# Performance work log

Hardware: AMD Instinct MI355X
Metric: run time of the kernel (lower is better)

The kernel has to match this reference:

```python
import jax, jax.numpy as jnp
import numpy as np

DIM = 1024
EXP = 4           # expansion_factor
NUM_EXPERTS = 4
BATCH, SEQ = 4, 4096


def setup_inputs() -> dict:
    key = jax.random.key(0)
    ks = jax.random.split(key, 6)
    x = jax.random.normal(ks[0], (BATCH, SEQ, DIM), dtype=jnp.float32)
    token_mask = jax.random.randint(ks[1], (BATCH, SEQ), 0, NUM_EXPERTS, dtype=jnp.int32)
    hid = DIM * EXP
    s1 = 1.0 / np.sqrt(DIM)
    s2 = 1.0 / np.sqrt(hid)
    # nn.Linear layout: weight [out_features, in_features]
    w1 = jax.random.uniform(ks[2], (hid, DIM), minval=-s1, maxval=s1, dtype=jnp.float32)
    b1 = jax.random.uniform(ks[3], (hid,), minval=-s1, maxval=s1, dtype=jnp.float32)
    w2 = jax.random.uniform(ks[4], (DIM, hid), minval=-s2, maxval=s2, dtype=jnp.float32)
    b2 = jax.random.uniform(ks[5], (DIM,), minval=-s2, maxval=s2, dtype=jnp.float32)
    return {"x": x, "w1": w1, "b1": b1, "w2": w2, "b2": b2, "token_mask": token_mask}


def _nested_ffn(x, w1, b1, w2, b2, token_mask):
    dim = x.shape[-1]            # in_features of proj1
    out_dim = w2.shape[0]        # out_features of proj2 (== dim)
    # Expert m uses the first D_m = width >> (E-1-m) features (matryoshka nesting).
    # Expand (proj1): truncating input features to D_m and doing a full GEMM is
    # exactly equivalent to zeroing features >= D_m, so we mask then do one GEMM.
    d_in = dim >> (NUM_EXPERTS - 1 - token_mask)             # [B,S]
    in_mask = jnp.arange(dim) < d_in[..., None]              # [B,S,dim]
    h = jnp.einsum('bsd,fd->bsf', jnp.where(in_mask, x, jnp.zeros((), x.dtype)), w1) + b1
    h = jax.nn.gelu(h, approximate=False)                    # torch nn.GELU() default = erf
    # Contract (proj2): expert m produces only the first D_m outputs (incl. bias),
    # padded with zeros -> compute full GEMM then mask outputs.
    d_out = out_dim >> (NUM_EXPERTS - 1 - token_mask)        # [B,S]
    out_mask = jnp.arange(out_dim) < d_out[..., None]        # [B,S,out_dim]
    y = jnp.einsum('bsf,df->bsd', h, w2) + b2
    return jnp.where(out_mask, y, jnp.zeros((), y.dtype))


def reference(x, w1, b1, w2, b2, token_mask):
    return _nested_ffn(x, w1, b1, w2, b2, token_mask)
```

## Files before the change

### kernel.cpp

```cpp
#include <hip/hip_runtime.h>
#include <hip/hip_bf16.h>


typedef __bf16 bf16x8 __attribute__((ext_vector_type(8)));
typedef float f32x4 __attribute__((ext_vector_type(4)));

#define M_TOK   16384
#define DIM     1024
#define HID     4096

#define META_TK    40
#define META_BLK   64
#define META_MAP   256
#define META_RT    2560

__device__ inline unsigned int pk_bf16(float a, float b) {
  unsigned int r;
  asm("v_cvt_pk_bf16_f32 %0, %1, %2" : "=v"(r) : "v"(a), "v"(b));
  return r;
}

__device__ inline float gelu_f(float v) {
  float v2 = v * v;
  float w = v * fmaf(0.10294324f, v2, 2.30220830f);
  float e = __builtin_amdgcn_exp2f(-w);
  return v * __builtin_amdgcn_rcpf(1.0f + e);
}

__device__ inline void async_copy16(const void* g, void* s) {
  __builtin_amdgcn_global_load_lds(
      (const __attribute__((address_space(1))) unsigned int*)g,
      (__attribute__((address_space(3))) unsigned int*)s,
      16, 0, 0);
}

template<int ROWS, int LDK>
__device__ inline void stage_tile(const unsigned short* __restrict__ g,
                                  int row0, int k0, char* lds) {
  const char* gbase = (const char*)g;
  int tid = threadIdx.x;
#pragma unroll
  for (int i = 0; i < ROWS / 32; ++i) {
    int q = i * 256 + tid;
    int r = q >> 3;
    int c = q & 7;
    int gc = c ^ (r & 7);
    const void* gp = gbase + ((size_t)(row0 + r) * LDK + (size_t)k0 + gc * 8) * 2;
    async_copy16(gp, lds + (size_t)q * 16);
  }
}

__global__ __launch_bounds__(1024) void sortw_kernel(
    const int* __restrict__ tm,
    const float* __restrict__ w1,
    const float* __restrict__ w2,
    int* __restrict__ meta,
    unsigned short* __restrict__ w1b,
    unsigned short* __restrict__ w2b) {
  int tid = threadIdx.x;
  if (blockIdx.x != 0) {
    size_t i = (size_t)(blockIdx.x - 1) * 4096 + tid * 4;
    const float* src;
    unsigned short* dst;
    if (i < (size_t)HID * DIM) { src = w1; dst = w1b; }
    else { src = w2 - (size_t)HID * DIM; dst = w2b - (size_t)HID * DIM; }
    float4 v = *(const float4*)(src + i);
    uint2 o;
    o.x = pk_bf16(v.x, v.y);
    o.y = pk_bf16(v.z, v.w);
    *(uint2*)(dst + i) = o;
    return;
  }

  __shared__ unsigned short rt[16384];
  __shared__ unsigned int w01[16], w23[16];
  __shared__ int sbase[4];
  __shared__ int cb[128];
  int lane = tid & 63, wv = tid >> 6;

  int c0 = 0, c1 = 0, c2 = 0, c3 = 0;
  unsigned int epack = 0;
  int4 tv[4];
#pragma unroll
  for (int j = 0; j < 4; ++j)
    tv[j] = *(const int4*)(tm + tid * 16 + j * 4);
#pragma unroll
  for (int j = 0; j < 4; ++j) {
    int e;
    e = tv[j].x; epack |= (unsigned)e << (2 * (4 * j + 0)); c0 += (e == 0); c1 += (e == 1); c2 += (e == 2); c3 += (e == 3);
    e = tv[j].y; epack |= (unsigned)e << (2 * (4 * j + 1)); c0 += (e == 0); c1 += (e == 1); c2 += (e == 2); c3 += (e == 3);
    e = tv[j].z; epack |= (unsigned)e << (2 * (4 * j + 2)); c0 += (e == 0); c1 += (e == 1); c2 += (e == 2); c3 += (e == 3);
    e = tv[j].w; epack |= (unsigned)e << (2 * (4 * j + 3)); c0 += (e == 0); c1 += (e == 1); c2 += (e == 2); c3 += (e == 3);
  }
  unsigned int p01 = (unsigned)c0 | ((unsigned)c1 << 16);
  unsigned int p23 = (unsigned)c2 | ((unsigned)c3 << 16);
  unsigned int i01 = p01, i23 = p23;
#pragma unroll
  for (int s = 1; s < 64; s <<= 1) {
    unsigned int t0 = __shfl_up(i01, s, 64);
    unsigned int t1 = __shfl_up(i23, s, 64);
    if (lane >= s) { i01 += t0; i23 += t1; }
  }
  if (lane == 63) { w01[wv] = i01; w23[wv] = i23; }
  unsigned int e01 = i01 - p01, e23 = i23 - p23;
  __syncthreads();
  if (tid < 16) {
    unsigned int a = w01[tid], b = w23[tid];
    unsigned int ia = a, ib = b;
#pragma unroll
    for (int s = 1; s < 16; s <<= 1) {
      unsigned int t0 = __shfl_up(ia, s, 64);
      unsigned int t1 = __shfl_up(ib, s, 64);
      if (tid >= s) { ia += t0; ib += t1; }
    }
    w01[tid] = ia - a;
    w23[tid] = ib - b;
    if (tid == 15) {
      int t0 = (int)(ia & 0xFFFF), t1 = (int)(ia >> 16), t2 = (int)(ib & 0xFFFF);
      sbase[0] = 0; sbase[1] = t0; sbase[2] = t0 + t1; sbase[3] = t0 + t1 + t2;
    }
  }
  __syncthreads();
  int off0 = sbase[0] + (int)((w01[wv] & 0xFFFF) + (e01 & 0xFFFF));
  int off1 = sbase[1] + (int)((w01[wv] >> 16) + (e01 >> 16));
  int off2 = sbase[2] + (int)((w23[wv] & 0xFFFF) + (e23 & 0xFFFF));
  int off3 = sbase[3] + (int)((w23[wv] >> 16) + (e23 >> 16));
#pragma unroll
  for (int j = 0; j < 16; ++j) {
    int e = (epack >> (2 * j)) & 3;
    int t = tid * 16 + j;
    int pos = (e == 0) ? off0++ : (e == 1) ? off1++ : (e == 2) ? off2++ : off3++;
    rt[pos] = (unsigned short)(t | (e << 14));
  }
  __syncthreads();

  if (tid < 128) {
    int last = tid * 128 + 127;
    int e = (last >= sbase[1]) + (last >= sbase[2]) + (last >= sbase[3]);
    cb[tid] = 1 << e;
    meta[META_BLK + tid] = 128 << e;
  }
  __syncthreads();
  if (tid < 8) {
    int k = tid;
    int* map = meta + META_MAP + k * 128;
    int Tk = 0;
    for (int j = 0; j < 16; ++j) Tk += cb[k + 8 * j];
    meta[META_TK + k] = Tk;
    int pos = 0, zpos = Tk;
    for (int j = 0; j < 16; ++j) {
      int s = k + 8 * j;
      int n = cb[s];
      for (int c = 0; c < n; ++c) map[pos++] = s * 8 + c;
      for (int c = n; c < 8; ++c) map[zpos++] = s * 8 + c;
    }
  }
  int* rowtok = meta + META_RT;
#pragma unroll
  for (int j = 0; j < 16; ++j)
    rowtok[j * 1024 + tid] = (int)rt[j * 1024 + tid];
}

__global__ void prepx_kernel(const float* __restrict__ x,
                             const int* __restrict__ meta,
                             unsigned short* __restrict__ xb) {
  int b = blockIdx.x;
  int tid = threadIdx.x;
  int mt = meta[META_RT + b];
  int t = mt & 0x3FFF;
  int din = 128 << (mt >> 14);
  int kb = meta[META_BLK + (b >> 7)];
  int d = tid * 4;
  if (d < kb) {
    uint2 o; o.x = 0; o.y = 0;
    if (d < din) {
      float4 v = *(const float4*)(x + (size_t)t * DIM + d);
      o.x = pk_bf16(v.x, v.y);
      o.y = pk_bf16(v.z, v.w);
    }
    *(uint2*)(xb + (size_t)b * DIM + d) = o;
  }
}

__global__ __launch_bounds__(256) void gemm1_kernel(
    const unsigned short* __restrict__ A,
    const unsigned short* __restrict__ B,
    const float* __restrict__ bias,
    const int* __restrict__ meta,
    unsigned short* __restrict__ H)
{
  constexpr int K = DIM, N = HID;
  __shared__ char smem[65536];
  int tid = threadIdx.x;
  int lane = tid & 63, quad = lane >> 4, l15 = lane & 15;
  int wave = tid >> 6, wm = wave & 1, wn = wave >> 1;
  int Bk = blockIdx.x & 7, ord = blockIdx.x >> 3;
  int rowblk = 127 - (ord >> 2);
  int row0 = rowblk * 128, col0 = (Bk * 4 + (ord & 3)) * 128;
  int kmax = meta[META_BLK + rowblk];

  int chb = (quad ^ (l15 & 7)) << 4;

  f32x4 acc[4][4] = {};

  stage_tile<128, K>(A, row0, 0, smem);
  stage_tile<128, K>(B, col0, 0, smem + 16384);

  int nt = kmax >> 6;
  for (int t = 0; t < nt; ++t) {
    char* buf = smem + ((t & 1) << 15);
    if (t + 1 < nt) {
      char* nbuf = smem + (((t + 1) & 1) << 15);
      int kn = (t + 1) << 6;
      stage_tile<128, K>(A, row0, kn, nbuf);
      stage_tile<128, K>(B, col0, kn, nbuf + 16384);
      asm volatile("s_waitcnt vmcnt(8)" ::: "memory");
    } else {
      asm volatile("s_waitcnt vmcnt(0)" ::: "memory");
    }
    __builtin_amdgcn_s_barrier();
    char* As = buf;
    char* Bs = buf + 16384;
#pragma unroll
    for (int kk = 0; kk < 2; ++kk) {
      int xo = chb ^ (kk << 6);
      bf16x8 af[4], bg[4];
#pragma unroll
      for (int mt = 0; mt < 4; ++mt)
        af[mt] = *(const bf16x8*)(As + (wm * 64 + mt * 16 + l15) * 128 + xo);
#pragma unroll
      for (int nt2 = 0; nt2 < 4; ++nt2)
        bg[nt2] = *(const bf16x8*)(Bs + (wn * 64 + nt2 * 16 + l15) * 128 + xo);
#pragma unroll
      for (int mt = 0; mt < 4; ++mt)
#pragma unroll
        for (int nt2 = 0; nt2 < 4; ++nt2)
          acc[mt][nt2] = __builtin_amdgcn_mfma_f32_16x16x32_bf16(
              bg[nt2], af[mt], acc[mt][nt2], 0, 0, 0);
    }
    __builtin_amdgcn_s_barrier();
  }

  int t_base = row0 + wm * 64;
  int f_base = col0 + wn * 64;
#pragma unroll
  for (int nt2 = 0; nt2 < 4; ++nt2) {
    int f0 = f_base + nt2 * 16 + quad * 4;
    float4 bv = *(const float4*)(bias + f0);
#pragma unroll
    for (int mt = 0; mt < 4; ++mt) {
      int t = t_base + mt * 16 + l15;
      float v0 = gelu_f(acc[mt][nt2][0] + bv.x);
      float v1 = gelu_f(acc[mt][nt2][1] + bv.y);
      float v2 = gelu_f(acc[mt][nt2][2] + bv.z);
      float v3 = gelu_f(acc[mt][nt2][3] + bv.w);
      uint2 p;
      p.x = pk_bf16(v0, v1);
      p.y = pk_bf16(v2, v3);
      *(uint2*)(H + (size_t)t * N + f0) = p;
    }
  }
}

__global__ __launch_bounds__(256) void gemm2_kernel(
    const unsigned short* __restrict__ A,
    const unsigned short* __restrict__ B,
    const float* __restrict__ bias,
    const int* __restrict__ meta,
    float* __restrict__ out)
{
  constexpr int K = HID, N = DIM;
  int Bk = blockIdx.x & 7, ord = blockIdx.x >> 3;
  int Tk = meta[META_TK + Bk];
  int mp = meta[META_MAP + Bk * 128 + ord];
  int row0 = (mp >> 3) * 128, col0 = (mp & 7) * 128;
  const int* rowtok = meta + META_RT;
  int tid = threadIdx.x;

  if (ord >= Tk) {
    float4 z = make_float4(0.f, 0.f, 0.f, 0.f);
#pragma unroll
    for (int i = 0; i < 16; ++i) {
      int idx = i * 256 + tid;
      int r = idx >> 5;
      int col = (idx & 31) * 4;
      int t = rowtok[row0 + r] & 0x3FFF;
      *(float4*)(out + (size_t)t * N + col0 + col) = z;
    }
    return;
  }

  __shared__ char smem[65536];
  int lane = tid & 63, quad = lane >> 4, l15 = lane & 15;
  int wave = tid >> 6, wm = wave & 1, wn = wave >> 1;
  int chb = (quad ^ (l15 & 7)) << 4;

  f32x4 acc[4][4] = {};

  stage_tile<128, K>(A, row0, 0, smem);
  stage_tile<128, K>(B, col0, 0, smem + 16384);

  constexpr int NT = K >> 6;
  for (int t = 0; t < NT; ++t) {
    char* buf = smem + ((t & 1) << 15);
    if (t + 1 < NT) {
      char* nbuf = smem + (((t + 1) & 1) << 15);
      int kn = (t + 1) << 6;
      stage_tile<128, K>(A, row0, kn, nbuf);
      stage_tile<128, K>(B, col0, kn, nbuf + 16384);
      asm volatile("s_waitcnt vmcnt(8)" ::: "memory");
    } else {
      asm volatile("s_waitcnt vmcnt(0)" ::: "memory");
    }
    __builtin_amdgcn_s_barrier();
    char* As = buf;
    char* Bs = buf + 16384;
#pragma unroll
    for (int kk = 0; kk < 2; ++kk) {
      int xo = chb ^ (kk << 6);
      bf16x8 af[4], bg[4];
#pragma unroll
      for (int mt = 0; mt < 4; ++mt)
        af[mt] = *(const bf16x8*)(As + (wm * 64 + mt * 16 + l15) * 128 + xo);
#pragma unroll
      for (int nt2 = 0; nt2 < 4; ++nt2)
        bg[nt2] = *(const bf16x8*)(Bs + (wn * 64 + nt2 * 16 + l15) * 128 + xo);
#pragma unroll
      for (int mt = 0; mt < 4; ++mt)
#pragma unroll
        for (int nt2 = 0; nt2 < 4; ++nt2)
          acc[mt][nt2] = __builtin_amdgcn_mfma_f32_16x16x32_bf16(
              bg[nt2], af[mt], acc[mt][nt2], 0, 0, 0);
    }
    __builtin_amdgcn_s_barrier();
  }

  int p_base = row0 + wm * 64;
  int d_base = col0 + wn * 64;
  float4 bv[4];
#pragma unroll
  for (int nt2 = 0; nt2 < 4; ++nt2)
    bv[nt2] = *(const float4*)(bias + d_base + nt2 * 16 + quad * 4);
#pragma unroll
  for (int mt = 0; mt < 4; ++mt) {
    int m2 = rowtok[p_base + mt * 16 + l15];
    int t = m2 & 0x3FFF;
    int dout = 128 << (m2 >> 14);
#pragma unroll
    for (int nt2 = 0; nt2 < 4; ++nt2) {
      int d0 = d_base + nt2 * 16 + quad * 4;
      bool ok = d0 < dout;
      float4 o;
      o.x = ok ? acc[mt][nt2][0] + bv[nt2].x : 0.0f;
      o.y = ok ? acc[mt][nt2][1] + bv[nt2].y : 0.0f;
      o.z = ok ? acc[mt][nt2][2] + bv[nt2].z : 0.0f;
      o.w = ok ? acc[mt][nt2][3] + bv[nt2].w : 0.0f;
      *(float4*)(out + (size_t)t * N + d0) = o;
    }
  }
}

extern "C" void kernel_launch(void* const* d_in, const int* in_sizes, int n_in,
                              void* d_out, int out_size, void* d_ws, size_t ws_size,
                              hipStream_t stream) {
  const float* x  = (const float*)d_in[0];
  const float* w1 = (const float*)d_in[1];
  const float* b1 = (const float*)d_in[2];
  const float* w2 = (const float*)d_in[3];
  const float* b2 = (const float*)d_in[4];
  const int*   tm = (const int*)d_in[5];
  float* out = (float*)d_out;

  char* ws = (char*)d_ws;
  int* meta = (int*)ws;
  unsigned short* xb  = (unsigned short*)(ws + 131072);
  unsigned short* w1b = (unsigned short*)(ws + 33685504);
  unsigned short* w2b = (unsigned short*)(ws + 42074112);
  unsigned short* hb  = (unsigned short*)(ws + 50462720);

  sortw_kernel<<<2049, 1024, 0, stream>>>(tm, w1, w2, meta, w1b, w2b);
  prepx_kernel<<<M_TOK, 256, 0, stream>>>(x, meta, xb);
  gemm1_kernel<<<4096, 256, 0, stream>>>(xb, w1b, b1, meta, hb);
  gemm2_kernel<<<1024, 256, 0, stream>>>(hb, w2b, b2, meta, out);
}
```

Measured before the change: 308.8 us.

## Enlarge gemm1 tiles to 256x256 with 512 threads and set MFMA priority

gemm1 moves from 128x128 tiles with 256 threads to 256x256 tiles with 512 threads (8 waves, each computing 128x64). It uses 128KB of LDS for double buffering and per-256-row K limits, stored in a new META_BLK2 table that prepx also reads. The goal is higher arithmetic intensity and fewer global loads per FLOP. It also hoists the B fragments, raises wave priority around the MFMA loop, and makes a small change to how gemm2 loads its A fragments. The costs are higher register pressure, lower occupancy, and coarser K truncation, since a 256-row block takes the largest expert width of any token in it.

```diff
diff --git a/kernel.cpp b/kernel.cpp
--- a/kernel.cpp
+++ b/kernel.cpp
@@ -11,6 +11,7 @@
 
 #define META_TK    40
 #define META_BLK   64
+#define META_BLK2  192
 #define META_MAP   256
 #define META_RT    2560
 
@@ -34,14 +35,14 @@
       16, 0, 0);
 }
 
-template<int ROWS, int LDK>
+template<int ROWS, int LDK, int THREADS>
 __device__ inline void stage_tile(const unsigned short* __restrict__ g,
                                   int row0, int k0, char* lds) {
   const char* gbase = (const char*)g;
   int tid = threadIdx.x;
 #pragma unroll
-  for (int i = 0; i < ROWS / 32; ++i) {
-    int q = i * 256 + tid;
+  for (int i = 0; i < ROWS * 8 / THREADS; ++i) {
+    int q = i * THREADS + tid;
     int r = q >> 3;
     int c = q & 7;
     int gc = c ^ (r & 7);
@@ -139,6 +140,11 @@
     int e = (last >= sbase[1]) + (last >= sbase[2]) + (last >= sbase[3]);
     cb[tid] = 1 << e;
     meta[META_BLK + tid] = 128 << e;
+  }
+  if (tid < 64) {
+    int last = tid * 256 + 255;
+    int e = (last >= sbase[1]) + (last >= sbase[2]) + (last >= sbase[3]);
+    meta[META_BLK2 + tid] = 128 << e;
   }
   __syncthreads();
   if (tid < 8) {
@@ -169,7 +175,7 @@
   int mt = meta[META_RT + b];
   int t = mt & 0x3FFF;
   int din = 128 << (mt >> 14);
-  int kb = meta[META_BLK + (b >> 7)];
+  int kb = meta[META_BLK2 + (b >> 8)];
   int d = tid * 4;
   if (d < kb) {
     uint2 o; o.x = 0; o.y = 0;
@@ -182,7 +188,7 @@
   }
 }
 
-__global__ __launch_bounds__(256) void gemm1_kernel(
+__global__ __launch_bounds__(512) void gemm1_kernel(
     const unsigned short* __restrict__ A,
     const unsigned short* __restrict__ B,
     const float* __restrict__ bias,
@@ -190,70 +196,75 @@
     unsigned short* __restrict__ H)
 {
   constexpr int K = DIM, N = HID;
-  __shared__ char smem[65536];
+  __shared__ char smem[131072];
   int tid = threadIdx.x;
   int lane = tid & 63, quad = lane >> 4, l15 = lane & 15;
-  int wave = tid >> 6, wm = wave & 1, wn = wave >> 1;
+  int wave = tid >> 6;
+  int wm = wave >> 2, wn = wave & 3;
   int Bk = blockIdx.x & 7, ord = blockIdx.x >> 3;
-  int rowblk = 127 - (ord >> 2);
-  int row0 = rowblk * 128, col0 = (Bk * 4 + (ord & 3)) * 128;
-  int kmax = meta[META_BLK + rowblk];
+  int rowblk = 63 - (ord >> 1);
+  int row0 = rowblk * 256, col0 = (Bk * 2 + (ord & 1)) * 256;
+  int kmax = meta[META_BLK2 + rowblk];
 
   int chb = (quad ^ (l15 & 7)) << 4;
 
-  f32x4 acc[4][4] = {};
-
-  stage_tile<128, K>(A, row0, 0, smem);
-  stage_tile<128, K>(B, col0, 0, smem + 16384);
+  f32x4 acc[8][4] = {};
+
+  stage_tile<256, K, 512>(A, row0, 0, smem);
+  stage_tile<256, K, 512>(B, col0, 0, smem + 32768);
 
   int nt = kmax >> 6;
   for (int t = 0; t < nt; ++t) {
-    char* buf = smem + ((t & 1) << 15);
+    char* buf = smem + ((t & 1) << 16);
     if (t + 1 < nt) {
-      char* nbuf = smem + (((t + 1) & 1) << 15);
+      char* nbuf = smem + (((t + 1) & 1) << 16);
       int kn = (t + 1) << 6;
-      stage_tile<128, K>(A, row0, kn, nbuf);
-      stage_tile<128, K>(B, col0, kn, nbuf + 16384);
+      stage_tile<256, K, 512>(A, row0, kn, nbuf);
+      stage_tile<256, K, 512>(B, col0, kn, nbuf + 32768);
       asm volatile("s_waitcnt vmcnt(8)" ::: "memory");
     } else {
       asm volatile("s_waitcnt vmcnt(0)" ::: "memory");
     }
     __builtin_amdgcn_s_barrier();
     char* As = buf;
-    char* Bs = buf + 16384;
-#pragma unroll
-    for (int kk = 0; kk < 2; ++kk) {
-      int xo = chb ^ (kk << 6);
-      bf16x8 af[4], bg[4];
-#pragma unroll
-      for (int mt = 0; mt < 4; ++mt)
-        af[mt] = *(const bf16x8*)(As + (wm * 64 + mt * 16 + l15) * 128 + xo);
-#pragma unroll
-      for (int nt2 = 0; nt2 < 4; ++nt2)
-        bg[nt2] = *(const bf16x8*)(Bs + (wn * 64 + nt2 * 16 + l15) * 128 + xo);
-#pragma unroll
-      for (int mt = 0; mt < 4; ++mt)
-#pragma unroll
-        for (int nt2 = 0; nt2 < 4; ++nt2)
-          acc[mt][nt2] = __builtin_amdgcn_mfma_f32_16x16x32_bf16(
-              bg[nt2], af[mt], acc[mt][nt2], 0, 0, 0);
-    }
+    char* Bs = buf + 32768;
+    bf16x8 bg[4][2];
+#pragma unroll
+    for (int nf = 0; nf < 4; ++nf)
+#pragma unroll
+      for (int kk = 0; kk < 2; ++kk)
+        bg[nf][kk] = *(const bf16x8*)(Bs + (wn * 64 + nf * 16 + l15) * 128 + (chb ^ (kk << 6)));
+    __builtin_amdgcn_s_setprio(1);
+#pragma unroll
+    for (int mf = 0; mf < 8; ++mf) {
+      bf16x8 a0 = *(const bf16x8*)(As + (wm * 128 + mf * 16 + l15) * 128 + chb);
+      bf16x8 a1 = *(const bf16x8*)(As + (wm * 128 + mf * 16 + l15) * 128 + (chb ^ 64));
+#pragma unroll
+      for (int nf = 0; nf < 4; ++nf)
+        acc[mf][nf] = __builtin_amdgcn_mfma_f32_16x16x32_bf16(
+            bg[nf][0], a0, acc[mf][nf], 0, 0, 0);
+#pragma unroll
+      for (int nf = 0; nf < 4; ++nf)
+        acc[mf][nf] = __builtin_amdgcn_mfma_f32_16x16x32_bf16(
+            bg[nf][1], a1, acc[mf][nf], 0, 0, 0);
+    }
+    __builtin_amdgcn_s_setprio(0);
     __builtin_amdgcn_s_barrier();
   }
 
-  int t_base = row0 + wm * 64;
+  int t_base = row0 + wm * 128;
   int f_base = col0 + wn * 64;
 #pragma unroll
-  for (int nt2 = 0; nt2 < 4; ++nt2) {
-    int f0 = f_base + nt2 * 16 + quad * 4;
+  for (int nf = 0; nf < 4; ++nf) {
+    int f0 = f_base + nf * 16 + quad * 4;
     float4 bv = *(const float4*)(bias + f0);
 #pragma unroll
-    for (int mt = 0; mt < 4; ++mt) {
-      int t = t_base + mt * 16 + l15;
-      float v0 = gelu_f(acc[mt][nt2][0] + bv.x);
-      float v1 = gelu_f(acc[mt][nt2][1] + bv.y);
-      float v2 = gelu_f(acc[mt][nt2][2] + bv.z);
-      float v3 = gelu_f(acc[mt][nt2][3] + bv.w);
+    for (int mf = 0; mf < 8; ++mf) {
+      int t = t_base + mf * 16 + l15;
+      float v0 = gelu_f(acc[mf][nf][0] + bv.x);
+      float v1 = gelu_f(acc[mf][nf][1] + bv.y);
+      float v2 = gelu_f(acc[mf][nf][2] + bv.z);
+      float v3 = gelu_f(acc[mf][nf][3] + bv.w);
       uint2 p;
       p.x = pk_bf16(v0, v1);
       p.y = pk_bf16(v2, v3);
@@ -297,8 +308,8 @@
 
   f32x4 acc[4][4] = {};
 
-  stage_tile<128, K>(A, row0, 0, smem);
-  stage_tile<128, K>(B, col0, 0, smem + 16384);
+  stage_tile<128, K, 256>(A, row0, 0, smem);
+  stage_tile<128, K, 256>(B, col0, 0, smem + 16384);
 
   constexpr int NT = K >> 6;
   for (int t = 0; t < NT; ++t) {
@@ -306,8 +317,8 @@
     if (t + 1 < NT) {
       char* nbuf = smem + (((t + 1) & 1) << 15);
       int kn = (t + 1) << 6;
-      stage_tile<128, K>(A, row0, kn, nbuf);
-      stage_tile<128, K>(B, col0, kn, nbuf + 16384);
+      stage_tile<128, K, 256>(A, row0, kn, nbuf);
+      stage_tile<128, K, 256>(B, col0, kn, nbuf + 16384);
       asm volatile("s_waitcnt vmcnt(8)" ::: "memory");
     } else {
       asm volatile("s_waitcnt vmcnt(0)" ::: "memory");
@@ -318,19 +329,21 @@
 #pragma unroll
     for (int kk = 0; kk < 2; ++kk) {
       int xo = chb ^ (kk << 6);
-      bf16x8 af[4], bg[4];
-#pragma unroll
-      for (int mt = 0; mt < 4; ++mt)
-        af[mt] = *(const bf16x8*)(As + (wm * 64 + mt * 16 + l15) * 128 + xo);
+      bf16x8 af[2], bg[4];
+#pragma unroll
+      for (int mt = 0; mt < 2; ++mt)
+        af[mt] = *(const bf16x8*)(As + (wm * 64 + (mt * 2 + 0) * 16 + l15) * 128 + xo);
 #pragma unroll
       for (int nt2 = 0; nt2 < 4; ++nt2)
         bg[nt2] = *(const bf16x8*)(Bs + (wn * 64 + nt2 * 16 + l15) * 128 + xo);
 #pragma unroll
-      for (int mt = 0; mt < 4; ++mt)
+      for (int mt = 0; mt < 4; ++mt) {
+        bf16x8 am = *(const bf16x8*)(As + (wm * 64 + mt * 16 + l15) * 128 + xo);
 #pragma unroll
         for (int nt2 = 0; nt2 < 4; ++nt2)
           acc[mt][nt2] = __builtin_amdgcn_mfma_f32_16x16x32_bf16(
-              bg[nt2], af[mt], acc[mt][nt2], 0, 0, 0);
+              bg[nt2], am, acc[mt][nt2], 0, 0, 0);
+      }
     }
     __builtin_amdgcn_s_barrier();
   }
@@ -380,6 +393,6 @@
 
   sortw_kernel<<<2049, 1024, 0, stream>>>(tm, w1, w2, meta, w1b, w2b);
   prepx_kernel<<<M_TOK, 256, 0, stream>>>(x, meta, xb);
-  gemm1_kernel<<<4096, 256, 0, stream>>>(xb, w1b, b1, meta, hb);
+  gemm1_kernel<<<1024, 512, 0, stream>>>(xb, w1b, b1, meta, hb);
   gemm2_kernel<<<1024, 256, 0, stream>>>(hb, w2b, b2, meta, out);
 }
```

New measurement: 328.4 us. +6.3%, slower.
